# Optimization experiments

Measured on AMD Instinct MI355X. Metric: run time of the kernel, lower is better.

Reference implementation:

```python
import jax, jax.numpy as jnp
import numpy as np

N = 20000
E = 320000
IN_DIM, HID, OUT_DIM = 32, 64, 4
HEADS = 4
NEG_SLOPE = 0.2


def _self_loops(src, dst):
    loop = jnp.arange(N, dtype=src.dtype)
    return jnp.concatenate([src, loop]), jnp.concatenate([dst, loop])


def gcn_conv(x, W, b, src, dst):
    h = x @ W                                            # [N, C]
    es, ed = _self_loops(src, dst)
    deg = jax.ops.segment_sum(jnp.ones_like(es, dtype=h.dtype), ed, num_segments=N)
    dinv = jnp.where(deg > 0, jax.lax.rsqrt(deg), 0.0)
    norm = dinv[es] * dinv[ed]                           # [E']
    out = jax.ops.segment_sum(h[es] * norm[:, None], ed, num_segments=N)
    return out + b


def gat_conv(x, W, att_src, att_dst, b, src, dst):
    # PyG GATConv: heads concat, self-loops, leaky_relu(0.2), softmax over incoming edges per dst
    H, C = att_src.shape
    h = (x @ W).reshape(N, H, C)                         # [N, H, C]
    a_s = jnp.sum(h * att_src, axis=-1)                  # [N, H]
    a_d = jnp.sum(h * att_dst, axis=-1)                  # [N, H]
    es, ed = _self_loops(src, dst)
    logits = jax.nn.leaky_relu(a_s[es] + a_d[ed], NEG_SLOPE)   # [E', H]
    m = jax.ops.segment_max(logits, ed, num_segments=N)
    expv = jnp.exp(logits - m[ed])
    denom = jax.ops.segment_sum(expv, ed, num_segments=N)
    alpha = expv / denom[ed]                             # [E', H]
    out = jax.ops.segment_sum(h[es] * alpha[:, :, None], ed, num_segments=N)
    return out.reshape(N, H * C) + b


def setup_inputs() -> dict:
    key = jax.random.key(0)
    ks = iter(jax.random.split(key, 32))
    s = 0.05
    def w(shape):
        return jax.random.normal(next(ks), shape, dtype=jnp.float32) * s
    inp = {}
    inp["x"] = jax.random.normal(next(ks), (N, IN_DIM), dtype=jnp.float32)
    inp["edge_index"] = jax.random.randint(next(ks), (2, E), 0, N, dtype=jnp.int32)
    # encoder1 GCN 32->64; encoder2 GCN 64->128; encoder3 GAT 128->128 x4 heads
    inp["w_e1"], inp["b_e1"] = w((IN_DIM, HID)), jnp.zeros((HID,), jnp.float32)
    inp["w_e2"], inp["b_e2"] = w((HID, 2 * HID)), jnp.zeros((2 * HID,), jnp.float32)
    inp["w_e3"] = w((2 * HID, HEADS * 2 * HID))
    inp["as_e3"], inp["ad_e3"] = w((HEADS, 2 * HID)), w((HEADS, 2 * HID))
    inp["b_e3"] = jnp.zeros((HEADS * 2 * HID,), jnp.float32)
    # decoder1 GCN 1024->128; decoder2 GCN 128->64; decoder3 GAT 64->64 x4 heads
    inp["w_d1"], inp["b_d1"] = w((HEADS * 2 * HID, 2 * HID)), jnp.zeros((2 * HID,), jnp.float32)
    inp["w_d2"], inp["b_d2"] = w((2 * HID, HID)), jnp.zeros((HID,), jnp.float32)
    inp["w_d3"] = w((HID, HEADS * HID))
    inp["as_d3"], inp["ad_d3"] = w((HEADS, HID)), w((HEADS, HID))
    inp["b_d3"] = jnp.zeros((HEADS * HID,), jnp.float32)
    # MLP head 256->256->128->4
    inp["w_fc1"], inp["b_fc1"] = w((4 * HID, 4 * HID)), jnp.zeros((4 * HID,), jnp.float32)
    inp["w_fc2"], inp["b_fc2"] = w((4 * HID, 2 * HID)), jnp.zeros((2 * HID,), jnp.float32)
    inp["w_fin"], inp["b_fin"] = w((2 * HID, OUT_DIM)), jnp.zeros((OUT_DIM,), jnp.float32)
    return inp


def reference(x, edge_index, w_e1, b_e1, w_e2, b_e2, w_e3, as_e3, ad_e3, b_e3,
              w_d1, b_d1, w_d2, b_d2, w_d3, as_d3, ad_d3, b_d3,
              w_fc1, b_fc1, w_fc2, b_fc2, w_fin, b_fin):
    src, dst = edge_index[0], edge_index[1]
    relu = jax.nn.relu
    x1 = relu(gcn_conv(x, w_e1, b_e1, src, dst))
    x2 = relu(gcn_conv(x1, w_e2, b_e2, src, dst))
    x3 = relu(gat_conv(x2, w_e3, as_e3, ad_e3, b_e3, src, dst))
    h = relu(gcn_conv(x3, w_d1, b_d1, src, dst)) + x2
    h = relu(gcn_conv(h, w_d2, b_d2, src, dst)) + x1
    h = relu(gat_conv(h, w_d3, as_d3, ad_d3, b_d3, src, dst))
    h = relu(h @ w_fc1 + b_fc1)
    h = relu(h @ w_fc2 + b_fc2)
    return h @ w_fin + b_fin
```

## Files before the change

kernel.cpp:

```cpp
#include <hip/hip_runtime.h>
#include <cstdint>
#include <cstddef>

static constexpr int Nn = 20000;
static constexpr int Ee = 320000;

typedef _Float16 half8 __attribute__((ext_vector_type(8)));
typedef float f32x4 __attribute__((ext_vector_type(4)));

__device__ __forceinline__ float lrelu02(float x){ return fmaxf(x, 0.2f*x); }
__device__ __forceinline__ float af(int x){ return __int_as_float(x); }

__device__ __forceinline__ void packhl(float v, unsigned short& h, unsigned short& l){
  _Float16 hh = (_Float16)v;
  _Float16 ll = (_Float16)((v - (float)hh) * 2048.0f);
  h = __builtin_bit_cast(unsigned short, hh);
  l = __builtin_bit_cast(unsigned short, ll);
}

__global__ void k_count(const int* __restrict__ dst, int* __restrict__ cnt){
  int e = blockIdx.x*256 + threadIdx.x;
  if (e < Ee) atomicAdd(&cnt[dst[e]], 1);
}

__global__ void k_scan(const int* __restrict__ cnt, int* __restrict__ row_start,
                       float* __restrict__ dinv){
  __shared__ int part[1024];
  int tid = threadIdx.x;
  const int PER = 20;
  int base = tid*PER;
  int s = 0;
  for (int i = 0; i < PER; ++i){ int idx = base+i; if (idx < Nn) s += cnt[idx]; }
  part[tid] = s; __syncthreads();
  for (int off = 1; off < 1024; off <<= 1){
    int v = (tid >= off) ? part[tid-off] : 0;
    __syncthreads();
    part[tid] += v;
    __syncthreads();
  }
  int run = (tid == 0) ? 0 : part[tid-1];
  for (int i = 0; i < PER; ++i){
    int idx = base+i;
    if (idx < Nn){
      row_start[idx] = run;
      int c = cnt[idx];
      run += c;
      dinv[idx] = rsqrtf((float)(c+1));
    }
  }
  if (tid == 1023) row_start[Nn] = run;
}

__global__ void k_scatter(const int* __restrict__ src, const int* __restrict__ dst,
                          const int* __restrict__ row_start, int* __restrict__ fill,
                          int* __restrict__ csr, const float* __restrict__ dinv,
                          int2* __restrict__ erec){
  int e = blockIdx.x*256 + threadIdx.x;
  if (e < Ee){
    int d = dst[e];
    int pos = row_start[d] + atomicAdd(&fill[d], 1);
    int u = src[e];
    csr[pos] = u;
    erec[pos] = make_int2(u, __float_as_int(dinv[u]));
  }
}

struct PrepArgs {
  const float *w_e1,*w_e2,*w_e3,*w_d1,*w_d2,*w_d3,*w_fc1,*w_fc2;
  unsigned short *p_e1,*p_e2,*p_e3,*p_d1,*p_d2,*p_d3,*p_fc1,*p_fc2;
  const float *as_e3,*ad_e3,*as_d3,*ad_d3;
  float *wsF_e3,*wdF_e3,*wsF_d3,*wdF_d3;
};

__device__ __forceinline__ void packw_one(const float* __restrict__ W,
                                          unsigned short* __restrict__ out,
                                          int i, int jlog, int K){
  int k = i >> jlog, col = i - (k << jlog);
  unsigned short h, l; packhl(W[i], h, l);
  size_t pos = ((size_t)((col>>4)*(K>>3) + (k>>3))*16 + (col&15))*8 + (k&7);
  out[pos] = h;
  out[pos + ((size_t)K << jlog)] = l;
}

__global__ void k_prep_weights(PrepArgs a){
  int i = blockIdx.x*256 + threadIdx.x;
  if      (i <   2048) packw_one(a.w_e1,  a.p_e1,  i,          6,  32);
  else if (i <  10240) packw_one(a.w_e2,  a.p_e2,  i-2048,     7,  64);
  else if (i <  75776) packw_one(a.w_e3,  a.p_e3,  i-10240,    9, 128);
  else if (i < 141312) packw_one(a.w_d1,  a.p_d1,  i-75776,    7, 512);
  else if (i < 149504) packw_one(a.w_d2,  a.p_d2,  i-141312,   6, 128);
  else if (i < 165888) packw_one(a.w_d3,  a.p_d3,  i-149504,   8,  64);
  else if (i < 231424) packw_one(a.w_fc1, a.p_fc1, i-165888,   8, 256);
  else if (i < 264192) packw_one(a.w_fc2, a.p_fc2, i-231424,   7, 256);
  else if (i < 264704){
    int t = i - 264192;
    int h = t >> 7, k = t & 127;
    float s = 0.f, d = 0.f;
    #pragma unroll 4
    for (int c = 0; c < 128; ++c){
      float wv = a.w_e3[(size_t)k*512 + h*128 + c];
      s = fmaf(wv, a.as_e3[h*128 + c], s);
      d = fmaf(wv, a.ad_e3[h*128 + c], d);
    }
    a.wsF_e3[h*128 + k] = s;
    a.wdF_e3[h*128 + k] = d;
  } else if (i < 264960){
    int t = i - 264704;
    int h = t >> 6, k = t & 63;
    float s = 0.f, d = 0.f;
    #pragma unroll 4
    for (int c = 0; c < 64; ++c){
      float wv = a.w_d3[(size_t)k*256 + h*64 + c];
      s = fmaf(wv, a.as_d3[h*64 + c], s);
      d = fmaf(wv, a.ad_d3[h*64 + c], d);
    }
    a.wsF_d3[h*64 + k] = s;
    a.wdF_d3[h*64 + k] = d;
  }
}

template<int C, int POST>
__global__ __launch_bounds__(256) void k_gcn_agg(
    const float* __restrict__ h, const float* __restrict__ dinv,
    const int* __restrict__ row_start, const int2* __restrict__ erec,
    const float* __restrict__ bias, const float* __restrict__ skip,
    float* __restrict__ outf, unsigned short* __restrict__ outp){
  int v = blockIdx.x*4 + (threadIdx.x >> 6);
  int lane = threadIdx.x & 63;
  int s = __builtin_amdgcn_readfirstlane(row_start[v]);
  int e = __builtin_amdgcn_readfirstlane(row_start[v+1]);
  float dv = dinv[v];
  const int c = (C==32) ? (lane & 31) : ((C==128) ? lane*2 : lane);

  float a0 = 0.f, a1 = 0.f;
  if constexpr (C == 32){
    int half = lane >> 5;
    int j = s + half;
    for (; j + 2 < e; j += 4){
      int2 r0 = erec[j], r1 = erec[j+2];
      float t0 = h[(size_t)r0.x*32 + c];
      float t1 = h[(size_t)r1.x*32 + c];
      a0 = fmaf(af(r0.y), t0, a0);
      a0 = fmaf(af(r1.y), t1, a0);
    }
    if (j < e){
      int2 r0 = erec[j];
      a0 = fmaf(af(r0.y), h[(size_t)r0.x*32 + c], a0);
    }
    a0 += __shfl_xor(a0, 32);
  } else if constexpr (C == 128){
    int j = s;
    for (; j + 4 <= e; j += 4){
      int2 r0 = erec[j], r1 = erec[j+1], r2 = erec[j+2], r3 = erec[j+3];
      float2 t0 = *(const float2*)&h[(size_t)r0.x*128 + c];
      float2 t1 = *(const float2*)&h[(size_t)r1.x*128 + c];
      float2 t2 = *(const float2*)&h[(size_t)r2.x*128 + c];
      float2 t3 = *(const float2*)&h[(size_t)r3.x*128 + c];
      a0=fmaf(af(r0.y),t0.x,a0); a1=fmaf(af(r0.y),t0.y,a1);
      a0=fmaf(af(r1.y),t1.x,a0); a1=fmaf(af(r1.y),t1.y,a1);
// ... 43 lines not shown
    float val = fmaf(a0, dv, h[(size_t)v*64 + c]*dv*dv);
    if constexpr (POST & 1){
      val = fmaxf(val + bias[c], 0.f) + skip[(size_t)v*64 + c];
    }
    if constexpr (POST & 2){
      unsigned short hh,ll; packhl(val,hh,ll);
      outp[(size_t)v*64 + c] = hh;
      outp[(size_t)v*64 + c + (size_t)Nn*64] = ll;
    } else {
      outf[(size_t)v*64 + c] = val;
    }
  } else {
    float val = fmaf(a0, dv, h[(size_t)v*32 + c]*dv*dv);
    if (lane < 32){
      unsigned short hh,ll; packhl(val,hh,ll);
      outp[(size_t)v*32 + c] = hh;
      outp[(size_t)v*32 + c + (size_t)Nn*32] = ll;
    }
  }
}

template<int INC>
__global__ __launch_bounds__(256) void k_attn_in(
    const float* __restrict__ X, const float* __restrict__ wsF, const float* __restrict__ wdF,
    float* __restrict__ aS, float* __restrict__ aD){
  int v = blockIdx.x*4 + (threadIdx.x >> 6);
  int lane = threadIdx.x & 63;
  float x0 = X[(size_t)v*INC + lane];
  float x1 = (INC == 128) ? X[(size_t)v*INC + 64 + lane] : 0.f;
  float s[4], d[4];
  #pragma unroll
  for (int h = 0; h < 4; ++h){
    s[h] = x0*wsF[h*INC + lane];
    d[h] = x0*wdF[h*INC + lane];
    if constexpr (INC == 128){
      s[h] = fmaf(x1, wsF[h*INC + 64 + lane], s[h]);
      d[h] = fmaf(x1, wdF[h*INC + 64 + lane], d[h]);
    }
  }
  #pragma unroll
  for (int off = 32; off; off >>= 1){
    #pragma unroll
    for (int h = 0; h < 4; ++h){
      s[h] += __shfl_xor(s[h], off);
      d[h] += __shfl_xor(d[h], off);
    }
  }
  if (lane == 0){
    *(float4*)&aS[v*4] = make_float4(s[0], s[1], s[2], s[3]);
    *(float4*)&aD[v*4] = make_float4(d[0], d[1], d[2], d[3]);
  }
}

__global__ __launch_bounds__(256) void k_gat_prep(
    const float* __restrict__ aS, const float* __restrict__ aD,
    const int* __restrict__ row_start, const int* __restrict__ csr,
    float4* __restrict__ alphaE, float4* __restrict__ fS4, float4* __restrict__ rin4){
  int v = blockIdx.x*4 + (threadIdx.x >> 6);
  int lane = threadIdx.x & 63;
  int s = row_start[v], e = row_start[v+1];

  float4 tD = *(const float4*)&aD[v*4];
  float ad0=tD.x, ad1=tD.y, ad2=tD.z, ad3=tD.w;
  float4 tS = *(const float4*)&aS[v*4];

  float sd0=0.f, sd1=0.f, sd2=0.f, sd3=0.f;
  for (int i = s + lane; i < e; i += 64){
    int u = csr[i];
    float4 a4 = *(const float4*)&aS[u*4];
    float f0 = __expf(lrelu02(a4.x+ad0));
    float f1 = __expf(lrelu02(a4.y+ad1));
    float f2 = __expf(lrelu02(a4.z+ad2));
    float f3 = __expf(lrelu02(a4.w+ad3));
    sd0 += f0; sd1 += f1; sd2 += f2; sd3 += f3;
    alphaE[i] = make_float4(f0, f1, f2, f3);
  }
  #pragma unroll
  for (int off = 32; off; off >>= 1){
    sd0 += __shfl_xor(sd0, off);
    sd1 += __shfl_xor(sd1, off);
    sd2 += __shfl_xor(sd2, off);
    sd3 += __shfl_xor(sd3, off);
  }
  if (lane == 0){
    float es0=__expf(lrelu02(tS.x+ad0)), es1=__expf(lrelu02(tS.y+ad1));
    float es2=__expf(lrelu02(tS.z+ad2)), es3=__expf(lrelu02(tS.w+ad3));
    fS4[v] = make_float4(es0, es1, es2, es3);
    rin4[v] = make_float4(1.f/(sd0+es0), 1.f/(sd1+es1), 1.f/(sd2+es2), 1.f/(sd3+es3));
  }
}

template<int INC>
__global__ __launch_bounds__(256) void k_gat_agg2(
    const float* __restrict__ X, const int* __restrict__ csr,
    const float4* __restrict__ alphaE, const float4* __restrict__ fS4,
    const float4* __restrict__ rin4, const int* __restrict__ row_start,
    unsigned short* __restrict__ outp){
  int v = blockIdx.x*4 + (threadIdx.x >> 6);
  int lane = threadIdx.x & 63;
  int s = __builtin_amdgcn_readfirstlane(row_start[v]);
  int e = __builtin_amdgcn_readfirstlane(row_start[v+1]);
  const int c2 = lane*2;

  float2 acc0={0,0}, acc1={0,0}, acc2={0,0}, acc3={0,0};
  float ac0=0.f, ac1=0.f, ac2=0.f, ac3=0.f;

  int j = s;
  for (; j + 4 <= e; j += 4){
    int u0=csr[j], u1=csr[j+1], u2=csr[j+2], u3=csr[j+3];
    float4 f0=alphaE[j], f1=alphaE[j+1], f2=alphaE[j+2], f3=alphaE[j+3];
    if constexpr (INC == 128){
      float2 x0 = *(const float2*)&X[(size_t)u0*128 + c2];
      float2 x1 = *(const float2*)&X[(size_t)u1*128 + c2];
      float2 x2 = *(const float2*)&X[(size_t)u2*128 + c2];
      float2 x3 = *(const float2*)&X[(size_t)u3*128 + c2];
      acc0.x=fmaf(f0.x,x0.x,acc0.x); acc0.y=fmaf(f0.x,x0.y,acc0.y);
      acc1.x=fmaf(f0.y,x0.x,acc1.x); acc1.y=fmaf(f0.y,x0.y,acc1.y);
      acc2.x=fmaf(f0.z,x0.x,acc2.x); acc2.y=fmaf(f0.z,x0.y,acc2.y);
      acc3.x=fmaf(f0.w,x0.x,acc3.x); acc3.y=fmaf(f0.w,x0.y,acc3.y);
      acc0.x=fmaf(f1.x,x1.x,acc0.x); acc0.y=fmaf(f1.x,x1.y,acc0.y);
      acc1.x=fmaf(f1.y,x1.x,acc1.x); acc1.y=fmaf(f1.y,x1.y,acc1.y);
      acc2.x=fmaf(f1.z,x1.x,acc2.x); acc2.y=fmaf(f1.z,x1.y,acc2.y);
      acc3.x=fmaf(f1.w,x1.x,acc3.x); acc3.y=fmaf(f1.w,x1.y,acc3.y);
      acc0.x=fmaf(f2.x,x2.x,acc0.x); acc0.y=fmaf(f2.x,x2.y,acc0.y);
      acc1.x=fmaf(f2.y,x2.x,acc1.x); acc1.y=fmaf(f2.y,x2.y,acc1.y);
      acc2.x=fmaf(f2.z,x2.x,acc2.x); acc2.y=fmaf(f2.z,x2.y,acc2.y);
      acc3.x=fmaf(f2.w,x2.x,acc3.x); acc3.y=fmaf(f2.w,x2.y,acc3.y);
      acc0.x=fmaf(f3.x,x3.x,acc0.x); acc0.y=fmaf(f3.x,x3.y,acc0.y);
      acc1.x=fmaf(f3.y,x3.x,acc1.x); acc1.y=fmaf(f3.y,x3.y,acc1.y);
      acc2.x=fmaf(f3.z,x3.x,acc2.x); acc2.y=fmaf(f3.z,x3.y,acc2.y);
      acc3.x=fmaf(f3.w,x3.x,acc3.x); acc3.y=fmaf(f3.w,x3.y,acc3.y);
    } else {
      float x0 = X[(size_t)u0*64 + lane];
      float x1 = X[(size_t)u1*64 + lane];
      float x2 = X[(size_t)u2*64 + lane];
      float x3 = X[(size_t)u3*64 + lane];
      ac0=fmaf(f0.x,x0,ac0); ac1=fmaf(f0.y,x0,ac1); ac2=fmaf(f0.z,x0,ac2); ac3=fmaf(f0.w,x0,ac3);
      ac0=fmaf(f1.x,x1,ac0); ac1=fmaf(f1.y,x1,ac1); ac2=fmaf(f1.z,x1,ac2); ac3=fmaf(f1.w,x1,ac3);
      ac0=fmaf(f2.x,x2,ac0); ac1=fmaf(f2.y,x2,ac1); ac2=fmaf(f2.z,x2,ac2); ac3=fmaf(f2.w,x2,ac3);
      ac0=fmaf(f3.x,x3,ac0); ac1=fmaf(f3.y,x3,ac1); ac2=fmaf(f3.z,x3,ac2); ac3=fmaf(f3.w,x3,ac3);
    }
  }
  for (; j < e; ++j){
    int u = csr[j];
    float4 f = alphaE[j];
    if constexpr (INC == 128){
      float2 xu = *(const float2*)&X[(size_t)u*128 + c2];
      acc0.x=fmaf(f.x,xu.x,acc0.x); acc0.y=fmaf(f.x,xu.y,acc0.y);
      acc1.x=fmaf(f.y,xu.x,acc1.x); acc1.y=fmaf(f.y,xu.y,acc1.y);
      acc2.x=fmaf(f.z,xu.x,acc2.x); acc2.y=fmaf(f.z,xu.y,acc2.y);
      acc3.x=fmaf(f.w,xu.x,acc3.x); acc3.y=fmaf(f.w,xu.y,acc3.y);
    } else {
      float xu = X[(size_t)u*64 + lane];
      ac0=fmaf(f.x,xu,ac0); ac1=fmaf(f.y,xu,ac1); ac2=fmaf(f.z,xu,ac2); ac3=fmaf(f.w,xu,ac3);
    }
  }

  float4 fs = fS4[v];
  float4 rv = rin4[v];

  if constexpr (INC == 128){
    float2 xv = *(const float2*)&X[(size_t)v*128 + c2];
    const size_t loOff = (size_t)Nn*512;
    float ox, oy; unsigned short h0,l0,h1,l1;
    ox=(acc0.x+fs.x*xv.x)*rv.x; oy=(acc0.y+fs.x*xv.y)*rv.x;
    packhl(ox,h0,l0); packhl(oy,h1,l1);
    *(unsigned int*)&outp[(size_t)v*512 +   0 + c2] = (unsigned)h0|((unsigned)h1<<16);
    *(unsigned int*)&outp[(size_t)v*512 +   0 + c2 + loOff] = (unsigned)l0|((unsigned)l1<<16);
    ox=(acc1.x+fs.y*xv.x)*rv.y; oy=(acc1.y+fs.y*xv.y)*rv.y;
    packhl(ox,h0,l0); packhl(oy,h1,l1);
    *(unsigned int*)&outp[(size_t)v*512 + 128 + c2] = (unsigned)h0|((unsigned)h1<<16);
    *(unsigned int*)&outp[(size_t)v*512 + 128 + c2 + loOff] = (unsigned)l0|((unsigned)l1<<16);
    ox=(acc2.x+fs.z*xv.x)*rv.z; oy=(acc2.y+fs.z*xv.y)*rv.z;
    packhl(ox,h0,l0); packhl(oy,h1,l1);
    *(unsigned int*)&outp[(size_t)v*512 + 256 + c2] = (unsigned)h0|((unsigned)h1<<16);
    *(unsigned int*)&outp[(size_t)v*512 + 256 + c2 + loOff] = (unsigned)l0|((unsigned)l1<<16);
    ox=(acc3.x+fs.w*xv.x)*rv.w; oy=(acc3.y+fs.w*xv.y)*rv.w;
    packhl(ox,h0,l0); packhl(oy,h1,l1);
    *(unsigned int*)&outp[(size_t)v*512 + 384 + c2] = (unsigned)h0|((unsigned)h1<<16);
    *(unsigned int*)&outp[(size_t)v*512 + 384 + c2 + loOff] = (unsigned)l0|((unsigned)l1<<16);
  } else {
    float xv = X[(size_t)v*64 + lane];
    const size_t loOff = (size_t)Nn*256;
    unsigned short hh,ll;
    float o;
    o = (ac0+fs.x*xv)*rv.x; packhl(o,hh,ll);
    outp[(size_t)v*256 +   0 + lane] = hh; outp[(size_t)v*256 +   0 + lane + loOff] = ll;
    o = (ac1+fs.y*xv)*rv.y; packhl(o,hh,ll);
    outp[(size_t)v*256 +  64 + lane] = hh; outp[(size_t)v*256 +  64 + lane + loOff] = ll;
    o = (ac2+fs.z*xv)*rv.z; packhl(o,hh,ll);
    outp[(size_t)v*256 + 128 + lane] = hh; outp[(size_t)v*256 + 128 + lane + loOff] = ll;
    o = (ac3+fs.w*xv)*rv.w; packhl(o,hh,ll);
    outp[(size_t)v*256 + 192 + lane] = hh; outp[(size_t)v*256 + 192 + lane + loOff] = ll;
  }
}

template<int K, int J, int Jh, int EPI>
__global__ __launch_bounds__(256) void k_gemm(
    const unsigned short* __restrict__ Ahi, int lda,
    const unsigned short* __restrict__ Wp,
    const float* __restrict__ bias,
    float* __restrict__ outf, unsigned short* __restrict__ outp){
  __shared__ unsigned short sAhi[2*64*8], sAlo[2*64*8];
  __shared__ unsigned short sBhi[4*64*8], sBlo[4*64*8];

  const int tid  = threadIdx.x;
  const int lane = tid & 63, w = tid >> 6;
  const int rh = w & 1, ch = w >> 1;
  const int rb = blockIdx.x;
  const int colbase = blockIdx.z*Jh + blockIdx.y*64;
  const int akoff   = blockIdx.z*K;
  const size_t AloOff = (size_t)Nn*lda;
  const size_t WloOff = (size_t)K*J;

  f32x4 accH0 = {0,0,0,0}, accH1 = {0,0,0,0};
  f32x4 accM0 = {0,0,0,0}, accM1 = {0,0,0,0};

  const int arow = tid >> 3;
  const int ak4  = (tid & 7) * 4;
  const int aw_idx = (((arow>>4)*4 + (ak4>>3))*16 + (arow&15))*8 + (ak4&4);
  const unsigned short* Ag = Ahi + (size_t)(rb*32 + arow)*lda + akoff + ak4;
  const int bcol = tid & 63;
  const int bkg  = tid >> 6;
  const int bw_idx = (((bcol>>4)*4 + bkg)*16 + (bcol&15))*8;
  const int cf_g  = (colbase>>4) + (bcol>>4);
  const size_t wbase = ((size_t)cf_g*(K/8)*16 + (size_t)(bcol&15))*8;

  #pragma unroll 1
  for (int ks = 0; ks < K/32; ++ks){
    if (ks) __syncthreads();
    {
      const unsigned short* p = Ag + ks*32;
      uint2 hv = *(const uint2*)p;
      uint2 lv = *(const uint2*)(p + AloOff);
      *(uint2*)&sAhi[aw_idx] = hv;
      *(uint2*)&sAlo[aw_idx] = lv;
    }
    {
      size_t goff = wbase + (size_t)(ks*4 + bkg)*16*8;
      uint4 hv = *(const uint4*)&Wp[goff];
      uint4 lv = *(const uint4*)&Wp[goff + WloOff];
      *(uint4*)&sBhi[bw_idx] = hv;
      *(uint4*)&sBlo[bw_idx] = lv;
    }
    __syncthreads();

    half8 aH = *(const half8*)&sAhi[(rh*64 + lane)*8];
    half8 aL = *(const half8*)&sAlo[(rh*64 + lane)*8];
    {
      int cf = ch*2;
      half8 bH = *(const half8*)&sBhi[(cf*64 + lane)*8];
      half8 bL = *(const half8*)&sBlo[(cf*64 + lane)*8];
      accH0 = __builtin_amdgcn_mfma_f32_16x16x32_f16(aH, bH, accH0, 0, 0, 0);
      accM0 = __builtin_amdgcn_mfma_f32_16x16x32_f16(aH, bL, accM0, 0, 0, 0);
      accM0 = __builtin_amdgcn_mfma_f32_16x16x32_f16(aL, bH, accM0, 0, 0, 0);
    }
    {
      int cf = ch*2 + 1;
      half8 bH = *(const half8*)&sBhi[(cf*64 + lane)*8];
      half8 bL = *(const half8*)&sBlo[(cf*64 + lane)*8];
      accH1 = __builtin_amdgcn_mfma_f32_16x16x32_f16(aH, bH, accH1, 0, 0, 0);
      accM1 = __builtin_amdgcn_mfma_f32_16x16x32_f16(aH, bL, accM1, 0, 0, 0);
      accM1 = __builtin_amdgcn_mfma_f32_16x16x32_f16(aL, bH, accM1, 0, 0, 0);
    }
  }

  #pragma unroll
  for (int q = 0; q < 2; ++q){
    int cf = ch*2 + q;
    int col = colbase + cf*16 + (lane & 15);
    float bv = (EPI >= 1) ? bias[col] : 0.f;
    const f32x4& aH = q ? accH1 : accH0;
    const f32x4& aM = q ? accM1 : accM0;
    #pragma unroll
    for (int r = 0; r < 4; ++r){
      int row = rb*32 + rh*16 + ((lane>>4)*4 + r);
      float v = aH[r] + aM[r]*(1.0f/2048.0f);
      if constexpr (EPI >= 1) v = fmaxf(v + bv, 0.f);
      if constexpr (EPI == 2){
        unsigned short hh, ll; packhl(v, hh, ll);
        outp[(size_t)row*J + col] = hh;
        outp[(size_t)row*J + col + (size_t)Nn*J] = ll;
      } else {
        outf[(size_t)row*J + col] = v;
      }
    }
  }
}

__global__ __launch_bounds__(256) void k_mm_fin(
    const float* __restrict__ A, const float* __restrict__ W,
    const float* __restrict__ bias, float* __restrict__ out){
  int row = blockIdx.x*4 + (threadIdx.x >> 6);
  int lane = threadIdx.x & 63;
  float a0 = A[(size_t)row*128 + lane];
  float a1 = A[(size_t)row*128 + 64 + lane];
  float4 w0 = ((const float4*)W)[lane];
  float4 w1 = ((const float4*)W)[64 + lane];
  float p0 = fmaf(a1, w1.x, a0*w0.x);
  float p1 = fmaf(a1, w1.y, a0*w0.y);
  float p2 = fmaf(a1, w1.z, a0*w0.z);
  float p3 = fmaf(a1, w1.w, a0*w0.w);
  #pragma unroll
  for (int off = 32; off; off >>= 1){
    p0 += __shfl_xor(p0, off);
    p1 += __shfl_xor(p1, off);
    p2 += __shfl_xor(p2, off);
    p3 += __shfl_xor(p3, off);
  }
  if (lane == 0){
    float4 bv = *(const float4*)bias;
    *(float4*)&out[(size_t)row*4] = make_float4(p0+bv.x, p1+bv.y, p2+bv.z, p3+bv.w);
  }
}

extern "C" void kernel_launch(void* const* d_in, const int* in_sizes, int n_in,
                              void* d_out, int out_size, void* d_ws, size_t ws_size,
                              hipStream_t stream){
  const float* x     = (const float*)d_in[0];
  const int*   ei    = (const int*)  d_in[1];
  const float* w_e1  = (const float*)d_in[2];
  const float* b_e1  = (const float*)d_in[3];
  const float* w_e2  = (const float*)d_in[4];
  const float* b_e2  = (const float*)d_in[5];
  const float* w_e3  = (const float*)d_in[6];
  const float* as_e3 = (const float*)d_in[7];
  const float* ad_e3 = (const float*)d_in[8];
  const float* b_e3  = (const float*)d_in[9];
  const float* w_d1  = (const float*)d_in[10];
  const float* b_d1  = (const float*)d_in[11];
  const float* w_d2  = (const float*)d_in[12];
  const float* b_d2  = (const float*)d_in[13];
  const float* w_d3  = (const float*)d_in[14];
  const float* as_d3 = (const float*)d_in[15];
  const float* ad_d3 = (const float*)d_in[16];
  const float* b_d3  = (const float*)d_in[17];
  const float* w_fc1 = (const float*)d_in[18];
  const float* b_fc1 = (const float*)d_in[19];
  const float* w_fc2 = (const float*)d_in[20];
  const float* b_fc2 = (const float*)d_in[21];
  const float* w_fin = (const float*)d_in[22];
  const float* b_fin = (const float*)d_in[23];

  char* ws = (char*)d_ws;
  size_t off = 0;
  auto alloc = [&](size_t bytes)->char*{
    char* p = ws + off;
    off += (bytes + 255) & ~size_t(255);
    return p;
  };
  int*   cnt       = (int*)  alloc((size_t)Nn*4);
  int*   fill      = (int*)  alloc((size_t)Nn*4);
  int*   row_start = (int*)  alloc((size_t)(Nn+1)*4);
  int*   csr       = (int*)  alloc((size_t)Ee*4);
  float* dinv      = (float*)alloc((size_t)Nn*4);
  int2*  erec      = (int2*) alloc((size_t)Ee*8);
  float4* alphaE   = (float4*)alloc((size_t)Ee*16);
  float4* fS4      = (float4*)alloc((size_t)Nn*16);
  float4* rin4     = (float4*)alloc((size_t)Nn*16);
  float* aSb       = (float*)alloc((size_t)Nn*16);
  float* aDb       = (float*)alloc((size_t)Nn*16);
  float* wsF_e3    = (float*)alloc(4*128*4);
  float* wdF_e3    = (float*)alloc(4*128*4);
  float* wsF_d3    = (float*)alloc(4*64*4);
  float* wdF_d3    = (float*)alloc(4*64*4);
  unsigned short* wp_e1  = (unsigned short*)alloc((size_t)32*64*4);
  unsigned short* wp_e2  = (unsigned short*)alloc((size_t)64*128*4);
  unsigned short* wp_e3  = (unsigned short*)alloc((size_t)128*512*4);
  unsigned short* wp_d1  = (unsigned short*)alloc((size_t)512*128*4);
  unsigned short* wp_d2  = (unsigned short*)alloc((size_t)128*64*4);
  unsigned short* wp_d3  = (unsigned short*)alloc((size_t)64*256*4);
  unsigned short* wp_fc1 = (unsigned short*)alloc((size_t)256*256*4);
  unsigned short* wp_fc2 = (unsigned short*)alloc((size_t)256*128*4);
  unsigned short* P0 = (unsigned short*)alloc((size_t)Nn*32*4);
  float* X1 = (float*)alloc((size_t)Nn*64*4);
  float* X2 = (float*)alloc((size_t)Nn*128*4);
  unsigned short* S1 = (unsigned short*)alloc((size_t)Nn*512*4);
  unsigned short* S2 = (unsigned short*)alloc((size_t)Nn*512*4);
  char*  S3 = alloc((size_t)Nn*128*4);

  const int* srcp = ei;
  const int* dstp = ei + Ee;

  hipMemsetAsync(cnt, 0, (size_t)(((size_t)Nn*4 + 255) & ~size_t(255)) + (size_t)Nn*4, stream);

  PrepArgs pa;
  pa.w_e1=w_e1; pa.w_e2=w_e2; pa.w_e3=w_e3; pa.w_d1=w_d1;
  pa.w_d2=w_d2; pa.w_d3=w_d3; pa.w_fc1=w_fc1; pa.w_fc2=w_fc2;
  pa.p_e1=wp_e1; pa.p_e2=wp_e2; pa.p_e3=wp_e3; pa.p_d1=wp_d1;
  pa.p_d2=wp_d2; pa.p_d3=wp_d3; pa.p_fc1=wp_fc1; pa.p_fc2=wp_fc2;
  pa.as_e3=as_e3; pa.ad_e3=ad_e3; pa.as_d3=as_d3; pa.ad_d3=ad_d3;
  pa.wsF_e3=wsF_e3; pa.wdF_e3=wdF_e3; pa.wsF_d3=wsF_d3; pa.wdF_d3=wdF_d3;
  k_prep_weights<<<1035, 256, 0, stream>>>(pa);

  k_count<<<(Ee+255)/256, 256, 0, stream>>>(dstp, cnt);
  k_scan<<<1, 1024, 0, stream>>>(cnt, row_start, dinv);
  k_scatter<<<(Ee+255)/256, 256, 0, stream>>>(srcp, dstp, row_start, fill, csr, dinv, erec);

  k_gcn_agg<32,2><<<Nn/4, 256, 0, stream>>>(x, dinv, row_start, erec, nullptr, nullptr, nullptr, P0);
  k_gemm<32,64,64,1><<<dim3(625,1,1), 256, 0, stream>>>(P0, 32, wp_e1, b_e1, X1, nullptr);
  k_gcn_agg<64,2><<<Nn/4, 256, 0, stream>>>(X1, dinv, row_start, erec, nullptr, nullptr, nullptr, (unsigned short*)S3);
  k_gemm<64,128,128,1><<<dim3(625,2,1), 256, 0, stream>>>((unsigned short*)S3, 64, wp_e2, b_e2, X2, nullptr);
  k_attn_in<128><<<Nn/4, 256, 0, stream>>>(X2, wsF_e3, wdF_e3, aSb, aDb);
  k_gat_prep<<<Nn/4, 256, 0, stream>>>(aSb, aDb, row_start, csr, alphaE, fS4, rin4);
  k_gat_agg2<128><<<Nn/4, 256, 0, stream>>>(X2, csr, alphaE, fS4, rin4, row_start, S1);
  k_gemm<128,512,128,2><<<dim3(625,2,4), 256, 0, stream>>>(S1, 512, wp_e3, b_e3, nullptr, S2);
  k_gemm<512,128,128,0><<<dim3(625,2,1), 256, 0, stream>>>(S2, 512, wp_d1, nullptr, (float*)S3, nullptr);
  k_gcn_agg<128,3><<<Nn/4, 256, 0, stream>>>((float*)S3, dinv, row_start, erec, b_d1, X2, nullptr, S1);
  k_gemm<128,64,64,0><<<dim3(625,1,1), 256, 0, stream>>>(S1, 128, wp_d2, nullptr, (float*)S2, nullptr);
  k_gcn_agg<64,1><<<Nn/4, 256, 0, stream>>>((float*)S2, dinv, row_start, erec, b_d2, X1, (float*)S3, nullptr);
  k_attn_in<64><<<Nn/4, 256, 0, stream>>>((float*)S3, wsF_d3, wdF_d3, aSb, aDb);
  k_gat_prep<<<Nn/4, 256, 0, stream>>>(aSb, aDb, row_start, csr, alphaE, fS4, rin4);
  k_gat_agg2<64><<<Nn/4, 256, 0, stream>>>((float*)S3, csr, alphaE, fS4, rin4, row_start, S1);
  k_gemm<64,256,64,2><<<dim3(625,1,4), 256, 0, stream>>>(S1, 256, wp_d3, b_d3, nullptr, S2);
  k_gemm<256,256,256,2><<<dim3(625,4,1), 256, 0, stream>>>(S2, 256, wp_fc1, b_fc1, nullptr, S1);
  k_gemm<256,128,128,1><<<dim3(625,2,1), 256, 0, stream>>>(S1, 256, wp_fc2, b_fc2, (float*)S2, nullptr);
  k_mm_fin<<<Nn/4, 256, 0, stream>>>((float*)S2, w_fin, b_fin, (float*)d_out);
}
```

Measured before the change: 350.2 us.

## Fuse GAT prep into aggregation, merge edge count into init, enlarge GEMM row tile

Folds the edge-count atomics into the weight-prep launch, which removes one kernel launch. Fuses the GAT softmax-numerator computation with the aggregation: per-edge exp weights are staged in shared memory per 64-edge chunk, so the alphaE/fS4/rin4 round trips through global memory go away. Changes the split-fp16 MFMA GEMM from 32-row to 64-row tiles, with each wave covering 16 rows by 64 columns and a clamped tail. This halves the grid and raises B-tile reuse, at the cost of more accumulator registers and a partial last tile.

Measured after the change: 349.3 us. No clear change (-0.3%).

```diff
diff --git a/kernel.cpp b/kernel.cpp
--- a/kernel.cpp
+++ b/kernel.cpp
@@ -16,11 +16,6 @@
   _Float16 ll = (_Float16)((v - (float)hh) * 2048.0f);
   h = __builtin_bit_cast(unsigned short, hh);
   l = __builtin_bit_cast(unsigned short, ll);
-}
-
-__global__ void k_count(const int* __restrict__ dst, int* __restrict__ cnt){
-  int e = blockIdx.x*256 + threadIdx.x;
-  if (e < Ee) atomicAdd(&cnt[dst[e]], 1);
 }
 
 __global__ void k_scan(const int* __restrict__ cnt, int* __restrict__ row_start,
@@ -70,6 +65,8 @@
   unsigned short *p_e1,*p_e2,*p_e3,*p_d1,*p_d2,*p_d3,*p_fc1,*p_fc2;
   const float *as_e3,*ad_e3,*as_d3,*ad_d3;
   float *wsF_e3,*wdF_e3,*wsF_d3,*wdF_d3;
+  const int* dst;
+  int* cnt;
 };
 
 __device__ __forceinline__ void packw_one(const float* __restrict__ W,
@@ -82,8 +79,14 @@
   out[pos + ((size_t)K << jlog)] = l;
 }
 
-__global__ void k_prep_weights(PrepArgs a){
-  int i = blockIdx.x*256 + threadIdx.x;
+__global__ void k_init(PrepArgs a){
+  int gi = blockIdx.x*256 + threadIdx.x;
+  if (gi >= 264960){
+    int e = gi - 264960;
+    if (e < Ee) atomicAdd(&a.cnt[a.dst[e]], 1);
+    return;
+  }
+  int i = gi;
   if      (i <   2048) packw_one(a.w_e1,  a.p_e1,  i,          6,  32);
   else if (i <  10240) packw_one(a.w_e2,  a.p_e2,  i-2048,     7,  64);
   else if (i <  75776) packw_one(a.w_e3,  a.p_e3,  i-10240,    9, 128);
@@ -104,7 +107,7 @@
     }
     a.wsF_e3[h*128 + k] = s;
     a.wdF_e3[h*128 + k] = d;
-  } else if (i < 264960){
+  } else {
     int t = i - 264704;
     int h = t >> 6, k = t & 63;
     float s = 0.f, d = 0.f;
@@ -254,29 +257,93 @@
   }
 }
 
-__global__ __launch_bounds__(256) void k_gat_prep(
+template<int INC>
+__global__ __launch_bounds__(256) void k_gat_fused(
+    const float* __restrict__ X, const int* __restrict__ csr,
     const float* __restrict__ aS, const float* __restrict__ aD,
-    const int* __restrict__ row_start, const int* __restrict__ csr,
-    float4* __restrict__ alphaE, float4* __restrict__ fS4, float4* __restrict__ rin4){
-  int v = blockIdx.x*4 + (threadIdx.x >> 6);
+    const int* __restrict__ row_start, unsigned short* __restrict__ outp){
+  __shared__ float4 sF[4][64];
+  int wv = threadIdx.x >> 6;
+  int v = blockIdx.x*4 + wv;
   int lane = threadIdx.x & 63;
-  int s = row_start[v], e = row_start[v+1];
+  int s = __builtin_amdgcn_readfirstlane(row_start[v]);
+  int e = __builtin_amdgcn_readfirstlane(row_start[v+1]);
+  const int c2 = lane*2;
 
   float4 tD = *(const float4*)&aD[v*4];
   float ad0=tD.x, ad1=tD.y, ad2=tD.z, ad3=tD.w;
   float4 tS = *(const float4*)&aS[v*4];
 
   float sd0=0.f, sd1=0.f, sd2=0.f, sd3=0.f;
-  for (int i = s + lane; i < e; i += 64){
-    int u = csr[i];
-    float4 a4 = *(const float4*)&aS[u*4];
-    float f0 = __expf(lrelu02(a4.x+ad0));
-    float f1 = __expf(lrelu02(a4.y+ad1));
-    float f2 = __expf(lrelu02(a4.z+ad2));
-    float f3 = __expf(lrelu02(a4.w+ad3));
-    sd0 += f0; sd1 += f1; sd2 += f2; sd3 += f3;
-    alphaE[i] = make_float4(f0, f1, f2, f3);
-  }
+  float2 acc0={0,0}, acc1={0,0}, acc2={0,0}, acc3={0,0};
+  float ac0=0.f, ac1=0.f, ac2=0.f, ac3=0.f;
+
+  for (int base = s; base < e; base += 64){
+    int i = base + lane;
+    float4 f = {0.f, 0.f, 0.f, 0.f};
+    if (i < e){
+      int u = csr[i];
+      float4 a4 = *(const float4*)&aS[u*4];
+      f.x = __expf(lrelu02(a4.x+ad0));
+      f.y = __expf(lrelu02(a4.y+ad1));
+      f.z = __expf(lrelu02(a4.z+ad2));
+      f.w = __expf(lrelu02(a4.w+ad3));
+      sd0 += f.x; sd1 += f.y; sd2 += f.z; sd3 += f.w;
+    }
+    sF[wv][lane] = f;
+    int cnt = min(64, e - base);
+    int j = 0;
+    for (; j + 4 <= cnt; j += 4){
+      int u0=csr[base+j], u1=csr[base+j+1], u2=csr[base+j+2], u3=csr[base+j+3];
+      float4 f0=sF[wv][j], f1=sF[wv][j+1], f2=sF[wv][j+2], f3=sF[wv][j+3];
+      if constexpr (INC == 128){
+        float2 x0 = *(const float2*)&X[(size_t)u0*128 + c2];
+        float2 x1 = *(const float2*)&X[(size_t)u1*128 + c2];
+        float2 x2 = *(const float2*)&X[(size_t)u2*128 + c2];
+        float2 x3 = *(const float2*)&X[(size_t)u3*128 + c2];
+        acc0.x=fmaf(f0.x,x0.x,acc0.x); acc0.y=fmaf(f0.x,x0.y,acc0.y);
+        acc1.x=fmaf(f0.y,x0.x,acc1.x); acc1.y=fmaf(f0.y,x0.y,acc1.y);
+        acc2.x=fmaf(f0.z,x0.x,acc2.x); acc2.y=fmaf(f0.z,x0.y,acc2.y);
+        acc3.x=fmaf(f0.w,x0.x,acc3.x); acc3.y=fmaf(f0.w,x0.y,acc3.y);
+        acc0.x=fmaf(f1.x,x1.x,acc0.x); acc0.y=fmaf(f1.x,x1.y,acc0.y);
+        acc1.x=fmaf(f1.y,x1.x,acc1.x); acc1.y=fmaf(f1.y,x1.y,acc1.y);
+        acc2.x=fmaf(f1.z,x1.x,acc2.x); acc2.y=fmaf(f1.z,x1.y,acc2.y);
+        acc3.x=fmaf(f1.w,x1.x,acc3.x); acc3.y=fmaf(f1.w,x1.y,acc3.y);
+        acc0.x=fmaf(f2.x,x2.x,acc0.x); acc0.y=fmaf(f2.x,x2.y,acc0.y);
+        acc1.x=fmaf(f2.y,x2.x,acc1.x); acc1.y=fmaf(f2.y,x2.y,acc1.y);
+        acc2.x=fmaf(f2.z,x2.x,acc2.x); acc2.y=fmaf(f2.z,x2.y,acc2.y);
+        acc3.x=fmaf(f2.w,x2.x,acc3.x); acc3.y=fmaf(f2.w,x2.y,acc3.y);
+        acc0.x=fmaf(f3.x,x3.x,acc0.x); acc0.y=fmaf(f3.x,x3.y,acc0.y);
+        acc1.x=fmaf(f3.y,x3.x,acc1.x); acc1.y=fmaf(f3.y,x3.y,acc1.y);
+        acc2.x=fmaf(f3.z,x3.x,acc2.x); acc2.y=fmaf(f3.z,x3.y,acc2.y);
+        acc3.x=fmaf(f3.w,x3.x,acc3.x); acc3.y=fmaf(f3.w,x3.y,acc3.y);
+      } else {
+        float x0 = X[(size_t)u0*64 + lane];
+        float x1 = X[(size_t)u1*64 + lane];
+        float x2 = X[(size_t)u2*64 + lane];
+        float x3 = X[(size_t)u3*64 + lane];
+        ac0=fmaf(f0.x,x0,ac0); ac1=fmaf(f0.y,x0,ac1); ac2=fmaf(f0.z,x0,ac2); ac3=fmaf(f0.w,x0,ac3);
+        ac0=fmaf(f1.x,x1,ac0); ac1=fmaf(f1.y,x1,ac1); ac2=fmaf(f1.z,x1,ac2); ac3=fmaf(f1.w,x1,ac3);
+        ac0=fmaf(f2.x,x2,ac0); ac1=fmaf(f2.y,x2,ac1); ac2=fmaf(f2.z,x2,ac2); ac3=fmaf(f2.w,x2,ac3);
+        ac0=fmaf(f3.x,x3,ac0); ac1=fmaf(f3.y,x3,ac1); ac2=fmaf(f3.z,x3,ac2); ac3=fmaf(f3.w,x3,ac3);
+      }
+    }
+    for (; j < cnt; ++j){
+      int u = csr[base+j];
+      float4 f4 = sF[wv][j];
+      if constexpr (INC == 128){
+        float2 xu = *(const float2*)&X[(size_t)u*128 + c2];
+        acc0.x=fmaf(f4.x,xu.x,acc0.x); acc0.y=fmaf(f4.x,xu.y,acc0.y);
+        acc1.x=fmaf(f4.y,xu.x,acc1.x); acc1.y=fmaf(f4.y,xu.y,acc1.y);
+        acc2.x=fmaf(f4.z,xu.x,acc2.x); acc2.y=fmaf(f4.z,xu.y,acc2.y);
+        acc3.x=fmaf(f4.w,xu.x,acc3.x); acc3.y=fmaf(f4.w,xu.y,acc3.y);
+      } else {
+        float xu = X[(size_t)u*64 + lane];
+        ac0=fmaf(f4.x,xu,ac0); ac1=fmaf(f4.y,xu,ac1); ac2=fmaf(f4.z,xu,ac2); ac3=fmaf(f4.w,xu,ac3);
+      }
+    }
+  }
+
   #pragma unroll
   for (int off = 32; off; off >>= 1){
     sd0 += __shfl_xor(sd0, off);
@@ -284,100 +351,27 @@
     sd2 += __shfl_xor(sd2, off);
     sd3 += __shfl_xor(sd3, off);
   }
-  if (lane == 0){
-    float es0=__expf(lrelu02(tS.x+ad0)), es1=__expf(lrelu02(tS.y+ad1));
-    float es2=__expf(lrelu02(tS.z+ad2)), es3=__expf(lrelu02(tS.w+ad3));
-    fS4[v] = make_float4(es0, es1, es2, es3);
-    rin4[v] = make_float4(1.f/(sd0+es0), 1.f/(sd1+es1), 1.f/(sd2+es2), 1.f/(sd3+es3));
-  }
-}
-
-template<int INC>
-__global__ __launch_bounds__(256) void k_gat_agg2(
-    const float* __restrict__ X, const int* __restrict__ csr,
-    const float4* __restrict__ alphaE, const float4* __restrict__ fS4,
-    const float4* __restrict__ rin4, const int* __restrict__ row_start,
-    unsigned short* __restrict__ outp){
-  int v = blockIdx.x*4 + (threadIdx.x >> 6);
-  int lane = threadIdx.x & 63;
-  int s = __builtin_amdgcn_readfirstlane(row_start[v]);
-  int e = __builtin_amdgcn_readfirstlane(row_start[v+1]);
-  const int c2 = lane*2;
-
-  float2 acc0={0,0}, acc1={0,0}, acc2={0,0}, acc3={0,0};
-  float ac0=0.f, ac1=0.f, ac2=0.f, ac3=0.f;
-
-  int j = s;
-  for (; j + 4 <= e; j += 4){
-    int u0=csr[j], u1=csr[j+1], u2=csr[j+2], u3=csr[j+3];
-    float4 f0=alphaE[j], f1=alphaE[j+1], f2=alphaE[j+2], f3=alphaE[j+3];
-    if constexpr (INC == 128){
-      float2 x0 = *(const float2*)&X[(size_t)u0*128 + c2];
-      float2 x1 = *(const float2*)&X[(size_t)u1*128 + c2];
-      float2 x2 = *(const float2*)&X[(size_t)u2*128 + c2];
-      float2 x3 = *(const float2*)&X[(size_t)u3*128 + c2];
-      acc0.x=fmaf(f0.x,x0.x,acc0.x); acc0.y=fmaf(f0.x,x0.y,acc0.y);
-      acc1.x=fmaf(f0.y,x0.x,acc1.x); acc1.y=fmaf(f0.y,x0.y,acc1.y);
-      acc2.x=fmaf(f0.z,x0.x,acc2.x); acc2.y=fmaf(f0.z,x0.y,acc2.y);
-      acc3.x=fmaf(f0.w,x0.x,acc3.x); acc3.y=fmaf(f0.w,x0.y,acc3.y);
-      acc0.x=fmaf(f1.x,x1.x,acc0.x); acc0.y=fmaf(f1.x,x1.y,acc0.y);
-      acc1.x=fmaf(f1.y,x1.x,acc1.x); acc1.y=fmaf(f1.y,x1.y,acc1.y);
-      acc2.x=fmaf(f1.z,x1.x,acc2.x); acc2.y=fmaf(f1.z,x1.y,acc2.y);
-      acc3.x=fmaf(f1.w,x1.x,acc3.x); acc3.y=fmaf(f1.w,x1.y,acc3.y);
-      acc0.x=fmaf(f2.x,x2.x,acc0.x); acc0.y=fmaf(f2.x,x2.y,acc0.y);
-      acc1.x=fmaf(f2.y,x2.x,acc1.x); acc1.y=fmaf(f2.y,x2.y,acc1.y);
-      acc2.x=fmaf(f2.z,x2.x,acc2.x); acc2.y=fmaf(f2.z,x2.y,acc2.y);
-      acc3.x=fmaf(f2.w,x2.x,acc3.x); acc3.y=fmaf(f2.w,x2.y,acc3.y);
-      acc0.x=fmaf(f3.x,x3.x,acc0.x); acc0.y=fmaf(f3.x,x3.y,acc0.y);
-      acc1.x=fmaf(f3.y,x3.x,acc1.x); acc1.y=fmaf(f3.y,x3.y,acc1.y);
-      acc2.x=fmaf(f3.z,x3.x,acc2.x); acc2.y=fmaf(f3.z,x3.y,acc2.y);
-      acc3.x=fmaf(f3.w,x3.x,acc3.x); acc3.y=fmaf(f3.w,x3.y,acc3.y);
-    } else {
-      float x0 = X[(size_t)u0*64 + lane];
-      float x1 = X[(size_t)u1*64 + lane];
-      float x2 = X[(size_t)u2*64 + lane];
-      float x3 = X[(size_t)u3*64 + lane];
-      ac0=fmaf(f0.x,x0,ac0); ac1=fmaf(f0.y,x0,ac1); ac2=fmaf(f0.z,x0,ac2); ac3=fmaf(f0.w,x0,ac3);
-      ac0=fmaf(f1.x,x1,ac0); ac1=fmaf(f1.y,x1,ac1); ac2=fmaf(f1.z,x1,ac2); ac3=fmaf(f1.w,x1,ac3);
-      ac0=fmaf(f2.x,x2,ac0); ac1=fmaf(f2.y,x2,ac1); ac2=fmaf(f2.z,x2,ac2); ac3=fmaf(f2.w,x2,ac3);
-      ac0=fmaf(f3.x,x3,ac0); ac1=fmaf(f3.y,x3,ac1); ac2=fmaf(f3.z,x3,ac2); ac3=fmaf(f3.w,x3,ac3);
-    }
-  }
-  for (; j < e; ++j){
-    int u = csr[j];
-    float4 f = alphaE[j];
-    if constexpr (INC == 128){
-      float2 xu = *(const float2*)&X[(size_t)u*128 + c2];
-      acc0.x=fmaf(f.x,xu.x,acc0.x); acc0.y=fmaf(f.x,xu.y,acc0.y);
-      acc1.x=fmaf(f.y,xu.x,acc1.x); acc1.y=fmaf(f.y,xu.y,acc1.y);
-      acc2.x=fmaf(f.z,xu.x,acc2.x); acc2.y=fmaf(f.z,xu.y,acc2.y);
-      acc3.x=fmaf(f.w,xu.x,acc3.x); acc3.y=fmaf(f.w,xu.y,acc3.y);
-    } else {
-      float xu = X[(size_t)u*64 + lane];
-      ac0=fmaf(f.x,xu,ac0); ac1=fmaf(f.y,xu,ac1); ac2=fmaf(f.z,xu,ac2); ac3=fmaf(f.w,xu,ac3);
-    }
-  }
-
-  float4 fs = fS4[v];
-  float4 rv = rin4[v];
+  float es0=__expf(lrelu02(tS.x+ad0)), es1=__expf(lrelu02(tS.y+ad1));
+  float es2=__expf(lrelu02(tS.z+ad2)), es3=__expf(lrelu02(tS.w+ad3));
+  float r0=1.f/(sd0+es0), r1=1.f/(sd1+es1), r2=1.f/(sd2+es2), r3=1.f/(sd3+es3);
 
   if constexpr (INC == 128){
     float2 xv = *(const float2*)&X[(size_t)v*128 + c2];
     const size_t loOff = (size_t)Nn*512;
     float ox, oy; unsigned short h0,l0,h1,l1;
-    ox=(acc0.x+fs.x*xv.x)*rv.x; oy=(acc0.y+fs.x*xv.y)*rv.x;
+    ox=(acc0.x+es0*xv.x)*r0; oy=(acc0.y+es0*xv.y)*r0;
     packhl(ox,h0,l0); packhl(oy,h1,l1);
     *(unsigned int*)&outp[(size_t)v*512 +   0 + c2] = (unsigned)h0|((unsigned)h1<<16);
     *(unsigned int*)&outp[(size_t)v*512 +   0 + c2 + loOff] = (unsigned)l0|((unsigned)l1<<16);
-    ox=(acc1.x+fs.y*xv.x)*rv.y; oy=(acc1.y+fs.y*xv.y)*rv.y;
+    ox=(acc1.x+es1*xv.x)*r1; oy=(acc1.y+es1*xv.y)*r1;
     packhl(ox,h0,l0); packhl(oy,h1,l1);
     *(unsigned int*)&outp[(size_t)v*512 + 128 + c2] = (unsigned)h0|((unsigned)h1<<16);
     *(unsigned int*)&outp[(size_t)v*512 + 128 + c2 + loOff] = (unsigned)l0|((unsigned)l1<<16);
-    ox=(acc2.x+fs.z*xv.x)*rv.z; oy=(acc2.y+fs.z*xv.y)*rv.z;
+    ox=(acc2.x+es2*xv.x)*r2; oy=(acc2.y+es2*xv.y)*r2;
     packhl(ox,h0,l0); packhl(oy,h1,l1);
     *(unsigned int*)&outp[(size_t)v*512 + 256 + c2] = (unsigned)h0|((unsigned)h1<<16);
     *(unsigned int*)&outp[(size_t)v*512 + 256 + c2 + loOff] = (unsigned)l0|((unsigned)l1<<16);
-    ox=(acc3.x+fs.w*xv.x)*rv.w; oy=(acc3.y+fs.w*xv.y)*rv.w;
+    ox=(acc3.x+es3*xv.x)*r3; oy=(acc3.y+es3*xv.y)*r3;
     packhl(ox,h0,l0); packhl(oy,h1,l1);
     *(unsigned int*)&outp[(size_t)v*512 + 384 + c2] = (unsigned)h0|((unsigned)h1<<16);
     *(unsigned int*)&outp[(size_t)v*512 + 384 + c2 + loOff] = (unsigned)l0|((unsigned)l1<<16);
@@ -386,13 +380,13 @@
     const size_t loOff = (size_t)Nn*256;
     unsigned short hh,ll;
     float o;
-    o = (ac0+fs.x*xv)*rv.x; packhl(o,hh,ll);
+    o = (ac0+es0*xv)*r0; packhl(o,hh,ll);
     outp[(size_t)v*256 +   0 + lane] = hh; outp[(size_t)v*256 +   0 + lane + loOff] = ll;
-    o = (ac1+fs.y*xv)*rv.y; packhl(o,hh,ll);
+    o = (ac1+es1*xv)*r1; packhl(o,hh,ll);
     outp[(size_t)v*256 +  64 + lane] = hh; outp[(size_t)v*256 +  64 + lane + loOff] = ll;
-    o = (ac2+fs.z*xv)*rv.z; packhl(o,hh,ll);
+    o = (ac2+es2*xv)*r2; packhl(o,hh,ll);
     outp[(size_t)v*256 + 128 + lane] = hh; outp[(size_t)v*256 + 128 + lane + loOff] = ll;
-    o = (ac3+fs.w*xv)*rv.w; packhl(o,hh,ll);
+    o = (ac3+es3*xv)*r3; packhl(o,hh,ll);
     outp[(size_t)v*256 + 192 + lane] = hh; outp[(size_t)v*256 + 192 + lane + loOff] = ll;
   }
 }
@@ -403,25 +397,25 @@
     const unsigned short* __restrict__ Wp,
     const float* __restrict__ bias,
     float* __restrict__ outf, unsigned short* __restrict__ outp){
-  __shared__ unsigned short sAhi[2*64*8], sAlo[2*64*8];
+  __shared__ unsigned short sAhi[4*64*8], sAlo[4*64*8];
   __shared__ unsigned short sBhi[4*64*8], sBlo[4*64*8];
 
   const int tid  = threadIdx.x;
   const int lane = tid & 63, w = tid >> 6;
-  const int rh = w & 1, ch = w >> 1;
   const int rb = blockIdx.x;
   const int colbase = blockIdx.z*Jh + blockIdx.y*64;
   const int akoff   = blockIdx.z*K;
   const size_t AloOff = (size_t)Nn*lda;
   const size_t WloOff = (size_t)K*J;
 
-  f32x4 accH0 = {0,0,0,0}, accH1 = {0,0,0,0};
-  f32x4 accM0 = {0,0,0,0}, accM1 = {0,0,0,0};
-
-  const int arow = tid >> 3;
-  const int ak4  = (tid & 7) * 4;
-  const int aw_idx = (((arow>>4)*4 + (ak4>>3))*16 + (arow&15))*8 + (ak4&4);
-  const unsigned short* Ag = Ahi + (size_t)(rb*32 + arow)*lda + akoff + ak4;
+  f32x4 accH[4] = {{0,0,0,0},{0,0,0,0},{0,0,0,0},{0,0,0,0}};
+  f32x4 accM[4] = {{0,0,0,0},{0,0,0,0},{0,0,0,0},{0,0,0,0}};
+
+  const int arow = tid >> 2;
+  const int akq  = (tid & 3) * 8;
+  int agrow = rb*64 + arow; if (agrow >= Nn) agrow = Nn - 1;
+  const unsigned short* Ag = Ahi + (size_t)agrow*lda + akoff + akq;
+  const int aw_idx = (((arow>>4)*4 + (akq>>3))*16 + (arow&15))*8;
   const int bcol = tid & 63;
   const int bkg  = tid >> 6;
   const int bw_idx = (((bcol>>4)*4 + bkg)*16 + (bcol&15))*8;
@@ -433,13 +427,13 @@
     if (ks) __syncthreads();
     {
       const unsigned short* p = Ag + ks*32;
-      uint2 hv = *(const uint2*)p;
-      uint2 lv = *(const uint2*)(p + AloOff);
-      *(uint2*)&sAhi[aw_idx] = hv;
-      *(uint2*)&sAlo[aw_idx] = lv;
+      uint4 hv = *(const uint4*)p;
+      uint4 lv = *(const uint4*)(p + AloOff);
+      *(uint4*)&sAhi[aw_idx] = hv;
+      *(uint4*)&sAlo[aw_idx] = lv;
     }
     {
-      size_t goff = wbase + (size_t)(ks*4 + bkg)*16*8;
+      size_t goff = wbase + (size_t)(ks*4 + bkg)*128;
       uint4 hv = *(const uint4*)&Wp[goff];
       uint4 lv = *(const uint4*)&Wp[goff + WloOff];
       *(uint4*)&sBhi[bw_idx] = hv;
@@ -447,44 +441,35 @@
     }
     __syncthreads();
 
-    half8 aH = *(const half8*)&sAhi[(rh*64 + lane)*8];
-    half8 aL = *(const half8*)&sAlo[(rh*64 + lane)*8];
-    {
-      int cf = ch*2;
+    half8 aH = *(const half8*)&sAhi[(w*64 + lane)*8];
+    half8 aL = *(const half8*)&sAlo[(w*64 + lane)*8];
+    #pragma unroll
+    for (int cf = 0; cf < 4; ++cf){
       half8 bH = *(const half8*)&sBhi[(cf*64 + lane)*8];
       half8 bL = *(const half8*)&sBlo[(cf*64 + lane)*8];
-      accH0 = __builtin_amdgcn_mfma_f32_16x16x32_f16(aH, bH, accH0, 0, 0, 0);
-      accM0 = __builtin_amdgcn_mfma_f32_16x16x32_f16(aH, bL, accM0, 0, 0, 0);
-      accM0 = __builtin_amdgcn_mfma_f32_16x16x32_f16(aL, bH, accM0, 0, 0, 0);
-    }
-    {
-      int cf = ch*2 + 1;
-      half8 bH = *(const half8*)&sBhi[(cf*64 + lane)*8];
-      half8 bL = *(const half8*)&sBlo[(cf*64 + lane)*8];
-      accH1 = __builtin_amdgcn_mfma_f32_16x16x32_f16(aH, bH, accH1, 0, 0, 0);
-      accM1 = __builtin_amdgcn_mfma_f32_16x16x32_f16(aH, bL, accM1, 0, 0, 0);
-      accM1 = __builtin_amdgcn_mfma_f32_16x16x32_f16(aL, bH, accM1, 0, 0, 0);
+      accH[cf] = __builtin_amdgcn_mfma_f32_16x16x32_f16(aH, bH, accH[cf], 0, 0, 0);
+      accM[cf] = __builtin_amdgcn_mfma_f32_16x16x32_f16(aH, bL, accM[cf], 0, 0, 0);
+      accM[cf] = __builtin_amdgcn_mfma_f32_16x16x32_f16(aL, bH, accM[cf], 0, 0, 0);
     }
   }
 
   #pragma unroll
-  for (int q = 0; q < 2; ++q){
-    int cf = ch*2 + q;
+  for (int cf = 0; cf < 4; ++cf){
     int col = colbase + cf*16 + (lane & 15);
     float bv = (EPI >= 1) ? bias[col] : 0.f;
-    const f32x4& aH = q ? accH1 : accH0;
-    const f32x4& aM = q ? accM1 : accM0;
     #pragma unroll
     for (int r = 0; r < 4; ++r){
-      int row = rb*32 + rh*16 + ((lane>>4)*4 + r);
-      float v = aH[r] + aM[r]*(1.0f/2048.0f);
-      if constexpr (EPI >= 1) v = fmaxf(v + bv, 0.f);
-      if constexpr (EPI == 2){
-        unsigned short hh, ll; packhl(v, hh, ll);
-        outp[(size_t)row*J + col] = hh;
-        outp[(size_t)row*J + col + (size_t)Nn*J] = ll;
-      } else {
-        outf[(size_t)row*J + col] = v;
+      int row = rb*64 + w*16 + ((lane>>4)*4 + r);
+      if (row < Nn){
+        float v = accH[cf][r] + accM[cf][r]*(1.0f/2048.0f);
+        if constexpr (EPI >= 1) v = fmaxf(v + bv, 0.f);
+        if constexpr (EPI == 2){
+          unsigned short hh, ll; packhl(v, hh, ll);
+          outp[(size_t)row*J + col] = hh;
+          outp[(size_t)row*J + col + (size_t)Nn*J] = ll;
+        } else {
+          outf[(size_t)row*J + col] = v;
+        }
       }
     }
   }
@@ -557,9 +542,6 @@
   int*   csr       = (int*)  alloc((size_t)Ee*4);
   float* dinv      = (float*)alloc((size_t)Nn*4);
   int2*  erec      = (int2*) alloc((size_t)Ee*8);
-  float4* alphaE   = (float4*)alloc((size_t)Ee*16);
-  float4* fS4      = (float4*)alloc((size_t)Nn*16);
-  float4* rin4     = (float4*)alloc((size_t)Nn*16);
   float* aSb       = (float*)alloc((size_t)Nn*16);
   float* aDb       = (float*)alloc((size_t)Nn*16);
   float* wsF_e3    = (float*)alloc(4*128*4);
@@ -593,29 +575,27 @@
   pa.p_d2=wp_d2; pa.p_d3=wp_d3; pa.p_fc1=wp_fc1; pa.p_fc2=wp_fc2;
   pa.as_e3=as_e3; pa.ad_e3=ad_e3; pa.as_d3=as_d3; pa.ad_d3=ad_d3;
   pa.wsF_e3=wsF_e3; pa.wdF_e3=wdF_e3; pa.wsF_d3=wsF_d3; pa.wdF_d3=wdF_d3;
-  k_prep_weights<<<1035, 256, 0, stream>>>(pa);
-
-  k_count<<<(Ee+255)/256, 256, 0, stream>>>(dstp, cnt);
+  pa.dst=dstp; pa.cnt=cnt;
+  k_init<<<2285, 256, 0, stream>>>(pa);
+
   k_scan<<<1, 1024, 0, stream>>>(cnt, row_start, dinv);
   k_scatter<<<(Ee+255)/256, 256, 0, stream>>>(srcp, dstp, row_start, fill, csr, dinv, erec);
 
   k_gcn_agg<32,2><<<Nn/4, 256, 0, stream>>>(x, dinv, row_start, erec, nullptr, nullptr, nullptr, P0);
-  k_gemm<32,64,64,1><<<dim3(625,1,1), 256, 0, stream>>>(P0, 32, wp_e1, b_e1, X1, nullptr);
+  k_gemm<32,64,64,1><<<dim3(313,1,1), 256, 0, stream>>>(P0, 32, wp_e1, b_e1, X1, nullptr);
   k_gcn_agg<64,2><<<Nn/4, 256, 0, stream>>>(X1, dinv, row_start, erec, nullptr, nullptr, nullptr, (unsigned short*)S3);
-  k_gemm<64,128,128,1><<<dim3(625,2,1), 256, 0, stream>>>((unsigned short*)S3, 64, wp_e2, b_e2, X2, nullptr);
+  k_gemm<64,128,128,1><<<dim3(313,2,1), 256, 0, stream>>>((unsigned short*)S3, 64, wp_e2, b_e2, X2, nullptr);
   k_attn_in<128><<<Nn/4, 256, 0, stream>>>(X2, wsF_e3, wdF_e3, aSb, aDb);
-  k_gat_prep<<<Nn/4, 256, 0, stream>>>(aSb, aDb, row_start, csr, alphaE, fS4, rin4);
-  k_gat_agg2<128><<<Nn/4, 256, 0, stream>>>(X2, csr, alphaE, fS4, rin4, row_start, S1);
-  k_gemm<128,512,128,2><<<dim3(625,2,4), 256, 0, stream>>>(S1, 512, wp_e3, b_e3, nullptr, S2);
-  k_gemm<512,128,128,0><<<dim3(625,2,1), 256, 0, stream>>>(S2, 512, wp_d1, nullptr, (float*)S3, nullptr);
+  k_gat_fused<128><<<Nn/4, 256, 0, stream>>>(X2, csr, aSb, aDb, row_start, S1);
+  k_gemm<128,512,128,2><<<dim3(313,2,4), 256, 0, stream>>>(S1, 512, wp_e3, b_e3, nullptr, S2);
+  k_gemm<512,128,128,0><<<dim3(313,2,1), 256, 0, stream>>>(S2, 512, wp_d1, nullptr, (float*)S3, nullptr);
   k_gcn_agg<128,3><<<Nn/4, 256, 0, stream>>>((float*)S3, dinv, row_start, erec, b_d1, X2, nullptr, S1);
-  k_gemm<128,64,64,0><<<dim3(625,1,1), 256, 0, stream>>>(S1, 128, wp_d2, nullptr, (float*)S2, nullptr);
+  k_gemm<128,64,64,0><<<dim3(313,1,1), 256, 0, stream>>>(S1, 128, wp_d2, nullptr, (float*)S2, nullptr);
   k_gcn_agg<64,1><<<Nn/4, 256, 0, stream>>>((float*)S2, dinv, row_start, erec, b_d2, X1, (float*)S3, nullptr);
   k_attn_in<64><<<Nn/4, 256, 0, stream>>>((float*)S3, wsF_d3, wdF_d3, aSb, aDb);
-  k_gat_prep<<<Nn/4, 256, 0, stream>>>(aSb, aDb, row_start, csr, alphaE, fS4, rin4);
-  k_gat_agg2<64><<<Nn/4, 256, 0, stream>>>((float*)S3, csr, alphaE, fS4, rin4, row_start, S1);
-  k_gemm<64,256,64,2><<<dim3(625,1,4), 256, 0, stream>>>(S1, 256, wp_d3, b_d3, nullptr, S2);
-  k_gemm<256,256,256,2><<<dim3(625,4,1), 256, 0, stream>>>(S2, 256, wp_fc1, b_fc1, nullptr, S1);
-  k_gemm<256,128,128,1><<<dim3(625,2,1), 256, 0, stream>>>(S1, 256, wp_fc2, b_fc2, (float*)S2, nullptr);
+  k_gat_fused<64><<<Nn/4, 256, 0, stream>>>((float*)S3, csr, aSb, aDb, row_start, S1);
+  k_gemm<64,256,64,2><<<dim3(313,1,4), 256, 0, stream>>>(S1, 256, wp_d3, b_d3, nullptr, S2);
+  k_gemm<256,256,256,2><<<dim3(313,4,1), 256, 0, stream>>>(S2, 256, wp_fc1, b_fc1, nullptr, S1);
+  k_gemm<256,128,128,1><<<dim3(313,2,1), 256, 0, stream>>>(S1, 256, wp_fc2, b_fc2, (float*)S2, nullptr);
   k_mm_fin<<<Nn/4, 256, 0, stream>>>((float*)S2, w_fin, b_fin, (float*)d_out);
 }
```
